# Kernel tuning notes

Measured on AMD Instinct MI355X. Metric: run time of the kernel, lower is better.

Reference implementation:

```python
import jax, jax.numpy as jnp
import numpy as np
from jax import lax


def conv2d(x, w, b, pad):
    # x: NCHW, w: OIHW
    out = lax.conv_general_dilated(x, w, (1, 1), [(pad, pad), (pad, pad)],
                                   dimension_numbers=('NCHW', 'OIHW', 'NCHW'))
    return out + b[None, :, None, None]


def traj_grid_sample(ps, gx, gy):
    """Faithful F.grid_sample (5D, trilinear, zeros padding, align_corners=False)
    applied to ps expanded along a depth axis of size L. Since every depth slice
    of the expanded input equals ps, we gather 2D from ps and fold the z-axis
    interpolation weights / bounds mask in analytically (no (B,C,L,H,W) expand).
    ps: (B,C,H,W); gx, gy: (B,L,H,W) pixel-coordinate flow fields."""
    B, C, H, W = ps.shape
    L = gx.shape[1]
    dt = ps.dtype
    # the original normalizes to [-1,1] assuming align_corners-style ranges
    gxn = gx / (W - 1) * 2 - 1
    gyn = gy / (H - 1) * 2 - 1
    gzn = jnp.arange(1, L + 1, dtype=dt) / (L - 1) * 2 - 1  # (L,)
    # torch grid_sample default align_corners=False unnormalization
    ix = ((gxn + 1) * W - 1) / 2
    iy = ((gyn + 1) * H - 1) / 2
    iz = jnp.broadcast_to((((gzn + 1) * L - 1) / 2)[None, :, None, None], ix.shape)
    x0 = jnp.floor(ix)
    y0 = jnp.floor(iy)
    z0 = jnp.floor(iz)
    bidx = jnp.arange(B)[:, None, None, None]
    out = jnp.zeros((B, L, H, W, C), dtype=dt)
    for dz in (0.0, 1.0):
        zc = z0 + dz
        wz = 1.0 - jnp.abs(iz - zc)
        mz = (zc >= 0) & (zc <= L - 1)
        for dy in (0.0, 1.0):
            yc = y0 + dy
            wy = 1.0 - jnp.abs(iy - yc)
            my = (yc >= 0) & (yc <= H - 1)
            yci = jnp.clip(yc, 0, H - 1).astype(jnp.int32)
            for dx in (0.0, 1.0):
                xc = x0 + dx
                wx = 1.0 - jnp.abs(ix - xc)
                mx = (xc >= 0) & (xc <= W - 1)
                xci = jnp.clip(xc, 0, W - 1).astype(jnp.int32)
                w = wz * wy * wx * (mz & my & mx).astype(dt)  # (B,L,H,W)
                val = ps[bidx, :, yci, xci]  # (B,L,H,W,C)
                out = out + val * w[..., None]
    return jnp.transpose(out, (0, 4, 1, 2, 3))  # (B,C,L,H,W)


def reference(x, prev_state, sub_w1, sub_b1, sub_w2, sub_b2,
              reset_w, reset_b, update_w, update_b, out_w, out_b,
              reset_ww, reset_wb, update_ww, update_wb, out_ww, out_wb):
    B, Ch, H, W = prev_state.shape
    L = sub_w2.shape[0] // 2
    # subCNN: flow generation
    s = jnp.concatenate([x, prev_state], axis=1)
    o = jax.nn.relu(conv2d(s, sub_w1, sub_b1, 2))
    o = jax.nn.relu(conv2d(o, sub_w2, sub_b2, 2))
    M = traj_grid_sample(prev_state, o[:, :L], o[:, L:])  # (B,Ch,L,H,W)
    Mf = M.reshape(B, Ch * L, H, W)  # view(B, C*L, H, W)
    update = jax.nn.sigmoid(conv2d(x, update_w, update_b, 1) + conv2d(Mf, update_ww, update_wb, 0))
    reset = jax.nn.sigmoid(conv2d(x, reset_w, reset_b, 1) + conv2d(Mf, reset_ww, reset_wb, 0))
    v = conv2d(x, out_w, out_b, 1) + reset * conv2d(Mf, out_ww, out_wb, 0)
    out_inputs = jnp.where(v >= 0, v, 0.2 * v)  # leaky_relu(0.2)
    return prev_state * update + out_inputs * (1.0 - update)


def setup_inputs() -> dict:
    key = jax.random.key(0)
    ks = jax.random.split(key, 12)
    B, Cin, Ch, L, H, W = 4, 8, 96, 13, 96, 96
    rn = lambda k, shape, s=0.05: jax.random.normal(k, shape, dtype=jnp.float32) * s
    z = lambda n: jnp.zeros((n,), jnp.float32)
    return {
        'x': rn(ks[0], (B, Cin, H, W), 1.0),
        'prev_state': rn(ks[1], (B, Ch, H, W), 1.0),
        'sub_w1': rn(ks[2], (32, Cin + Ch, 5, 5)), 'sub_b1': z(32),
        'sub_w2': rn(ks[3], (2 * L, 32, 5, 5)), 'sub_b2': z(2 * L),
        'reset_w': rn(ks[4], (Ch, Cin, 3, 3)), 'reset_b': z(Ch),
        'update_w': rn(ks[5], (Ch, Cin, 3, 3)), 'update_b': z(Ch),
        'out_w': rn(ks[6], (Ch, Cin, 3, 3)), 'out_b': z(Ch),
        'reset_ww': rn(ks[7], (Ch, Ch * L, 1, 1)), 'reset_wb': z(Ch),
        'update_ww': rn(ks[8], (Ch, Ch * L, 1, 1)), 'update_wb': z(Ch),
        'out_ww': rn(ks[9], (Ch, Ch * L, 1, 1)), 'out_wb': z(Ch),
    }
```

## Files before the change

### kernel.cpp

```cpp
#include <hip/hip_runtime.h>
#include <hip/hip_bf16.h>

#define HW 9216

typedef unsigned short ushort;
typedef unsigned int   uint;
typedef __attribute__((ext_vector_type(4))) float f32x4;
typedef __attribute__((ext_vector_type(2))) uint  u32x2;
typedef __attribute__((ext_vector_type(4))) uint  u32x4;
typedef __attribute__((ext_vector_type(4))) int   i32x4;
typedef __attribute__((ext_vector_type(8))) short s16x8;
typedef __attribute__((ext_vector_type(8))) _Float16 f16x8;

__device__ float  g_o1[4*32*HW];
__device__ float  g_q [2*4*26*HW];
__device__ __align__(16) _Float16 g_hh[4*(size_t)HW*96];
__device__ __align__(16) ushort g_chi[4*(size_t)HW*128];
__device__ __align__(16) ushort g_clo[4*(size_t)HW*128];
__device__ __align__(16) ushort g_w1b[28*4*2048];
__device__ __align__(16) ushort g_b[18*39*512];
__device__ __align__(16) float  g_urv[2304*288*16];

__device__ __forceinline__ ushort f2b(float f){
  uint x = __float_as_uint(f);
  return (ushort)((x + 0x7FFFu + ((x >> 16) & 1u)) >> 16);
}
__device__ __forceinline__ float b2f(ushort h){
  return __uint_as_float(((uint)h) << 16);
}

__global__ void pack_b_k(const float* __restrict__ uww, const float* __restrict__ rww,
                         const float* __restrict__ vww){
  int i = blockIdx.x*256 + threadIdx.x;
  if (i >= 3*96*1248) return;
  int gate = i / (96*1248); int rem = i % (96*1248);
  int oc = rem / 1248;      int kp = rem % 1248;
  int l = kp / 96, c = kp % 96;
  const float* src = (gate == 0) ? uww : ((gate == 1) ? rww : vww);
  float v = src[oc*1248 + c*13 + l];
  int n  = gate*96 + oc;
  int nt = n >> 4, nl = n & 15;
  int kb = kp >> 5, kk = kp & 31;
  g_b[(nt*39 + kb)*512 + ((kk >> 3)*16 + nl)*8 + (kk & 7)] = f2b(v);
}

__global__ void pack_w1b_k(const float* __restrict__ w1){
  int i = blockIdx.x*256 + threadIdx.x;
  if (i >= 25*4*1024) return;
  int tap = i >> 12;
  int cb  = (i >> 10) & 3;
  int oc  = (i >> 5) & 31;
  int kk  = i & 31;
  int ci  = cb*32 + kk;
  float w = (ci < 104) ? w1[oc*2600 + ci*25 + tap] : 0.f;
  ushort h = f2b(w);
  float rem = w - b2f(h);
  int base = ((tap*4 + cb) << 11) + (oc >> 4)*512 + (oc & 15)*32 + kk;
  g_w1b[base]        = h;
  g_w1b[base + 1024] = f2b(rem);
}

__global__ __launch_bounds__(256) void transpose_k(const float* __restrict__ hp,
                                                   const float* __restrict__ x){
  __shared__ float tile[32][33];
  int s0 = blockIdx.x*32;
  int b  = blockIdx.z;
  int t  = threadIdx.x;
  if (blockIdx.y < 3){
    int c0 = blockIdx.y*32;
    for (int i = t; i < 32*32; i += 256){
      int c = i >> 5, s = i & 31;
      tile[c][s] = hp[((size_t)(b*96 + c0 + c))*HW + s0 + s];
    }
    __syncthreads();
    for (int i = t; i < 32*32; i += 256){
      int s = i >> 5, c = i & 31;
      float v = tile[c][s];
      size_t px = (size_t)b*HW + s0 + s;
      g_hh[px*96 + c0 + c] = (_Float16)v;
      ushort h = f2b(v);
      g_chi[px*128 + 8 + c0 + c] = h;
      g_clo[px*128 + 8 + c0 + c] = f2b(v - b2f(h));
    }
  } else {
    for (int i = t; i < 8*32; i += 256){
      int c = i >> 5, s = i & 31;
      tile[c][s] = x[((size_t)(b*8 + c))*HW + s0 + s];
    }
    __syncthreads();
    for (int i = t; i < 32*8; i += 256){
      int s = i >> 3, c = i & 7;
      float v = tile[c][s];
      size_t px = (size_t)b*HW + s0 + s;
      ushort h = f2b(v);
      g_chi[px*128 + c] = h;
      g_clo[px*128 + c] = f2b(v - b2f(h));
    }
  }
}

__global__ __launch_bounds__(256) void conv1_mfma_k(const float* __restrict__ b1){
  __shared__ __align__(16) ushort sh[2*160*128];
  int t = threadIdx.x;
  int w = t >> 6, lane = t & 63;
  int nl = lane & 15, q = lane >> 4;
  int rt = blockIdx.x / 6, ct = blockIdx.x % 6;
  int b  = blockIdx.z;
  int r0 = rt*4, c0 = ct*16;
  const size_t pbase = (size_t)b*HW;

  #pragma unroll
  for (int i = 0; i < 20; i++){
    int idx = i*256 + t;
    int half = (i >= 10) ? 1 : 0;
    int rem = idx - half*2560;
    int px = rem >> 4, ci = rem & 15;
    int cs = ci ^ (px & 15);
    int r = px / 20, c = px - r*20;
    int gr = r0 + r - 2, gc = c0 + c - 2;
    f32x4 v = (f32x4){0.f,0.f,0.f,0.f};
    if ((unsigned)gr < 96u && (unsigned)gc < 96u){
      const ushort* src = half ? g_clo : g_chi;
      v = *(const f32x4*)(src + ((pbase + (size_t)(gr*96 + gc)) << 7) + cs*8);
    }
    *(f32x4*)((char*)sh + (size_t)idx*16) = v;
  }
  __syncthreads();

  int kxA[7], kyA[7], tpA[7];
  #pragma unroll
  for (int i = 0; i < 7; i++){
    int tp  = 7*w + i;
    int tpc = (tp > 24) ? 24 : tp;
    kyA[i] = tpc / 5;
    kxA[i] = tpc - kyA[i]*5;
    tpA[i] = tp;
  }
  int foff = nl*32 + q*8;

  f32x4 acc[4][2];
  #pragma unroll
  for (int mr = 0; mr < 4; mr++){
    acc[mr][0] = (f32x4){0.f,0.f,0.f,0.f};
    acc[mr][1] = (f32x4){0.f,0.f,0.f,0.f};
  }

  for (int cb = 0; cb < 4; cb++){
    const ushort* bpc = g_w1b + ((size_t)cb << 11);
    s16x8 bq[3][4];
#define LOADB(slot, i) { const ushort* bp = bpc + ((size_t)tpA[i] << 13); \
    bq[slot][0] = *(const s16x8*)(bp + foff); \
    bq[slot][1] = *(const s16x8*)(bp + 512 + foff); \
    bq[slot][2] = *(const s16x8*)(bp + 1024 + foff); \
    bq[slot][3] = *(const s16x8*)(bp + 1536 + foff); }
    LOADB(0, 0); LOADB(1, 1);

    #pragma unroll
    for (int i = 0; i < 7; i++){
      if (i < 5) LOADB((i + 2) % 3, i + 2);
      int ky = kyA[i], kx = kxA[i];
      int chq = cb*4 + q;
      s16x8 ah[4], al[4];
      #pragma unroll
      for (int mr = 0; mr < 4; mr++){
        int px  = (mr + ky)*20 + kx + nl;
        int off = px*256 + (((chq ^ (px & 15))) << 4);
        ah[mr] = *(const s16x8*)((const char*)sh + off);
        al[mr] = *(const s16x8*)((const char*)sh + 40960 + off);
      }
      const int cur = i % 3;
      #pragma unroll
      for (int mr = 0; mr < 4; mr++){
        acc[mr][0] = __builtin_amdgcn_mfma_f32_16x16x32_bf16(ah[mr], bq[cur][0], acc[mr][0], 0,0,0);
        acc[mr][1] = __builtin_amdgcn_mfma_f32_16x16x32_bf16(ah[mr], bq[cur][1], acc[mr][1], 0,0,0);
      }
      #pragma unroll
      for (int mr = 0; mr < 4; mr++){
        acc[mr][0] = __builtin_amdgcn_mfma_f32_16x16x32_bf16(al[mr], bq[cur][0], acc[mr][0], 0,0,0);
        acc[mr][1] = __builtin_amdgcn_mfma_f32_16x16x32_bf16(al[mr], bq[cur][1], acc[mr][1], 0,0,0);
      }
      #pragma unroll
      for (int mr = 0; mr < 4; mr++){
        acc[mr][0] = __builtin_amdgcn_mfma_f32_16x16x32_bf16(ah[mr], bq[cur][2], acc[mr][0], 0,0,0);
        acc[mr][1] = __builtin_amdgcn_mfma_f32_16x16x32_bf16(ah[mr], bq[cur][3], acc[mr][1], 0,0,0);
      }
    }
#undef LOADB
  }

  __syncthreads();
  float* red = (float*)sh;
  #pragma unroll
  for (int mr = 0; mr < 4; mr++)
    #pragma unroll
    for (int nt = 0; nt < 2; nt++)
      *(f32x4*)&red[(((mr*2 + nt)*4 + w) << 8) + lane*4] = acc[mr][nt];
  __syncthreads();

  int mr = w;
  #pragma unroll
  for (int nt = 0; nt < 2; nt++){
    f32x4 s = (f32x4){0.f,0.f,0.f,0.f};
    #pragma unroll
    for (int ww = 0; ww < 4; ww++)
      s += *(f32x4*)&red[(((mr*2 + nt)*4 + ww) << 8) + lane*4];
    int oc = nt*16 + nl;
    float bias = b1[oc];
    s.x = fmaxf(s.x + bias, 0.f); s.y = fmaxf(s.y + bias, 0.f);
    s.z = fmaxf(s.z + bias, 0.f); s.w = fmaxf(s.w + bias, 0.f);
    *(f32x4*)(g_o1 + ((size_t)(b*32 + oc))*HW + (size_t)(r0 + mr)*96 + c0 + q*4) = s;
  }
}

__global__ __launch_bounds__(256) void conv2_k(const float* __restrict__ wt2,
                                               const float* __restrict__ b2){
  __shared__ __align__(16) float in_sh[8][20][24];
  __shared__ __align__(16) float w_sh[8][25][32];
  int tile = blockIdx.x;
  int kg   = blockIdx.y;
  int b    = blockIdx.z;
  int row0 = (tile / 6) * 16, col0 = (tile % 6) * 16;
  int t = threadIdx.x;
  int og  = t >> 5;
  int pos = t & 31;
  int row = pos >> 1, x0 = (pos & 1)*8;

  float acc[8][4];
  #pragma unroll
  for (int j = 0; j < 8; j++)
    #pragma unroll
    for (int o = 0; o < 4; o++) acc[j][o] = 0.f;

  for (int cc = 0; cc < 2; cc++){
    __syncthreads();
    for (int idx = t; idx < 8*20*24; idx += 256){
      int i = idx / 480, rem = idx % 480;
      int r = rem / 24, c = rem % 24;
      int gr = row0 + r - 2, gc = col0 + c - 2;
      float v = 0.f;
      if ((unsigned)gr < 96u && (unsigned)gc < 96u){
        int ci = kg*16 + cc*8 + i;
        v = g_o1[(b*32 + ci)*HW + gr*96 + gc];
      }
      in_sh[i][r][c] = v;
    }
    for (int idx = t; idx < 8*25*32; idx += 256){
      int i = idx / 800, rem = idx % 800;
      int tap = rem / 32, oc = rem % 32;
      int ci = kg*16 + cc*8 + i;
      w_sh[i][tap][oc] = (oc < 26) ? wt2[oc*800 + ci*25 + tap] : 0.f;
    }
    __syncthreads();

    for (int i = 0; i < 8; i++){
      #pragma unroll
      for (int ky = 0; ky < 5; ky++){
        const float* rp = &in_sh[i][row + ky][x0];
        f32x4 s0 = *(const f32x4*)(rp);
        f32x4 s1 = *(const f32x4*)(rp + 4);
        f32x4 s2 = *(const f32x4*)(rp + 8);
        float seg[12] = {s0.x,s0.y,s0.z,s0.w, s1.x,s1.y,s1.z,s1.w, s2.x,s2.y,s2.z,s2.w};
        #pragma unroll
        for (int kx = 0; kx < 5; kx++){
          f32x4 wv = *(const f32x4*)&w_sh[i][ky*5 + kx][og*4];
          #pragma unroll
          for (int j = 0; j < 8; j++){
            float a = seg[kx + j];
            acc[j][0] += a*wv.x; acc[j][1] += a*wv.y;
            acc[j][2] += a*wv.z; acc[j][3] += a*wv.w;
          }
        }
      }
    }
  }

  int rg = row0 + row, cg = col0 + x0;
  #pragma unroll
  for (int o = 0; o < 4; o++){
    int slot = og*4 + o;
    if (slot < 26){
      float bias = (kg == 0) ? b2[slot] : 0.f;
      float* d = g_q + (size_t)kg*4*26*HW + ((size_t)(b*26 + slot))*HW + rg*96 + cg;
      #pragma unroll
      for (int j = 0; j < 8; j++) d[j] = acc[j][o] + bias;
    }
  }
}

__global__ __launch_bounds__(256) void gemm_k(){
  __shared__ __align__(16) ushort Bsh[18*512];
  __shared__ __align__(16) float cw4[12][64][4];
  __shared__ __align__(16) int   co4[12][64][4];
  int t = threadIdx.x;
  int w = t >> 6, lane = t & 63;
  int nl = lane & 15, quad = lane >> 4;
  int blk = blockIdx.x;
  int b   = blk / 144;
  int pbase0 = (blk % 144) * 64;
  int pt  = blk*4 + w;

  const int NQ = 4*26*HW;
  for (int idx = t; idx < 768; idx += 256){
    int l = idx >> 6, m = idx & 63;
    int p = pbase0 + m;
    float gx = fmaxf(g_q[(b*26 + l     )*HW + p] + g_q[NQ + (b*26 + l     )*HW + p], 0.f);
    float gy = fmaxf(g_q[(b*26 + 13 + l)*HW + p] + g_q[NQ + (b*26 + 13 + l)*HW + p], 0.f);
    float ix = gx * (96.f/95.f) - 0.5f;
    float iy = gy * (96.f/95.f) - 0.5f;
    float iz = (float)(l+1) * (13.f/12.f) - 0.5f;
    float z0 = floorf(iz);
    float zf = 0.f;
    #pragma unroll
    for (int dz = 0; dz < 2; dz++){
      float zc = z0 + (float)dz;
      float wz = 1.f - fabsf(iz - zc);
      if (zc >= 0.f && zc <= 12.f) zf += wz;
    }
    float x0f = floorf(ix), y0f = floorf(iy);
    #pragma unroll
    for (int dy = 0; dy < 2; dy++){
      float yc = y0f + (float)dy;
      float wy = 1.f - fabsf(iy - yc);
      bool  my = (yc >= 0.f) && (yc <= 95.f);
      int  yci = min(max((int)yc, 0), 95);
      #pragma unroll
      for (int dx = 0; dx < 2; dx++){
        float xc = x0f + (float)dx;
        float wx = 1.f - fabsf(ix - xc);
        bool  mx = (xc >= 0.f) && (xc <= 95.f);
        int  xci = min(max((int)xc, 0), 95);
        cw4[l][m][dy*2+dx] = (mx && my) ? zf*wy*wx : 0.f;
        co4[l][m][dy*2+dx] = yci*96 + xci;
      }
    }
  }

  f32x4 acc[18];
  #pragma unroll
  for (int nt = 0; nt < 18; nt++) acc[nt] = (f32x4){0.f,0.f,0.f,0.f};

  const u32x2* Bg8 = reinterpret_cast<const u32x2*>(g_b);
  const _Float16* hb = g_hh + (size_t)b*HW*96 + quad*8;
  int mloc = w*16 + nl;

  f16x8 gA[4], gB[4];
  f32x4 wA, wB;
  u32x2 sA[9], sB[9];

  #pragma unroll
  for (int u = 0; u < 9; u++){
    int idx8 = u*256 + t;
    sA[u] = Bg8[((idx8 >> 7)*39 + 0)*128 + (idx8 & 127)];
  }
  __syncthreads();

  {
    wA = *(const f32x4*)cw4[0][mloc];
    i32x4 ov_ = *(const i32x4*)co4[0][mloc];
    gA[0] = *(const f16x8*)(hb + (size_t)ov_.x*96);
    gA[1] = *(const f16x8*)(hb + (size_t)ov_.y*96);
    gA[2] = *(const f16x8*)(hb + (size_t)ov_.z*96);
    gA[3] = *(const f16x8*)(hb + (size_t)ov_.w*96);
  }
  int ln = 0, k3n = 1;

#define BODY(KB, GC, WC, GN, WN, SC, SN, PF) { \
  if (PF){ \
    _Pragma("unroll") \
    for (int u = 0; u < 9; u++){ \
      int idx8 = u*256 + t; \
      SN[u] = Bg8[((idx8 >> 7)*39 + (KB) + 1)*128 + (idx8 & 127)]; \
    } \
    WN = *(const f32x4*)cw4[ln][mloc]; \
    i32x4 ov_ = *(const i32x4*)co4[ln][mloc]; \
    const _Float16* hc_ = hb + k3n*32; \
    GN[0] = *(const f16x8*)(hc_ + (size_t)ov_.x*96); \
    GN[1] = *(const f16x8*)(hc_ + (size_t)ov_.y*96); \
    GN[2] = *(const f16x8*)(hc_ + (size_t)ov_.z*96); \
    GN[3] = *(const f16x8*)(hc_ + (size_t)ov_.w*96); \
    k3n++; if (k3n == 3){ k3n = 0; ln++; } \
  } \
  _Pragma("unroll") \
  for (int u = 0; u < 9; u++){ \
    int idx8 = u*256 + t; \
    *(u32x2*)((char*)Bsh + idx8*8) = SC[u]; \
  } \
  float av[8]; \
  _Pragma("unroll") \
  for (int j = 0; j < 8; j++) \
    av[j] = WC.x*(float)GC[0][j] + WC.y*(float)GC[1][j] \
          + WC.z*(float)GC[2][j] + WC.w*(float)GC[3][j]; \
  union { u32x4 u4; s16x8 s8v; } cv_; \
  cv_.u4.x = (uint)f2b(av[0]) | ((uint)f2b(av[1]) << 16); \
  cv_.u4.y = (uint)f2b(av[2]) | ((uint)f2b(av[3]) << 16); \
  cv_.u4.z = (uint)f2b(av[4]) | ((uint)f2b(av[5]) << 16); \
  cv_.u4.w = (uint)f2b(av[6]) | ((uint)f2b(av[7]) << 16); \
  asm volatile("s_waitcnt lgkmcnt(0)" ::: "memory"); \
  __builtin_amdgcn_s_barrier(); \
  asm volatile("" ::: "memory"); \
  _Pragma("unroll") \
  for (int nt = 0; nt < 18; nt++){ \
    s16x8 bf = *(const s16x8*)((const char*)Bsh + nt*1024 + lane*16); \
    acc[nt] = __builtin_amdgcn_mfma_f32_16x16x32_bf16(cv_.s8v, bf, acc[nt], 0, 0, 0); \
  } \
  asm volatile("" ::: "memory"); \
  __builtin_amdgcn_s_barrier(); \
  asm volatile("" ::: "memory"); \
}

  for (int kb = 0; kb < 34; kb += 2){
    BODY(kb,     gA, wA, gB, wB, sA, sB, 1);
    BODY(kb + 1, gB, wB, gA, wA, sB, sA, 1);
  }
  BODY(34, gA, wA, gB, wB, sA, sB, 1);
  BODY(35, gB, wB, gA, wA, sB, sA, 0);
#undef BODY

  float* dst = g_urv + (size_t)pt*4608;
  #pragma unroll
  for (int nt = 0; nt < 18; nt++)
    *(f32x4*)&dst[(nt*16 + nl)*16 + quad*4] = acc[nt];
}

__global__ __launch_bounds__(256) void gate_k(const float* __restrict__ x,
                        const float* __restrict__ hp,
                        const float* __restrict__ uw, const float* __restrict__ ub,
                        const float* __restrict__ rw, const float* __restrict__ rb,
                        const float* __restrict__ vw, const float* __restrict__ vb,
                        const float* __restrict__ uwb, const float* __restrict__ rwb,
                        const float* __restrict__ vwb, float* __restrict__ out){
  int p  = blockIdx.x*256 + threadIdx.x;
  int oc = blockIdx.y;
  int b  = blockIdx.z;
  int h = p/96, w = p%96;
  float xU = ub[oc], xR = rb[oc], xV = vb[oc];
  const float* xb = x + b*8*HW;
  for (int ky = 0; ky < 3; ky++){
    int r = h+ky-1;
    if ((unsigned)r >= 96u) continue;
    for (int kx = 0; kx < 3; kx++){
      int c = w+kx-1;
      if ((unsigned)c >= 96u) continue;
      int off = r*96 + c;
      int wo  = ky*3 + kx;
      #pragma unroll
      for (int ic = 0; ic < 8; ic++){
        float a = xb[ic*HW + off];
        xU += a * uw[oc*72 + ic*9 + wo];
        xR += a * rw[oc*72 + ic*9 + wo];
        xV += a * vw[oc*72 + ic*9 + wo];
      }
    }
  }
  int pt = b*576 + (p >> 4), px = p & 15;
  const float* ur = g_urv + (size_t)pt*4608 + px;
  float gU = ur[(0*96 + oc)*16] + uwb[oc];
  float gR = ur[(1*96 + oc)*16] + rwb[oc];
  float gV = ur[(2*96 + oc)*16] + vwb[oc];
  float u = 1.f / (1.f + __expf(-(xU + gU)));
  float r = 1.f / (1.f + __expf(-(xR + gR)));
  float v = xV + r * gV;
  float oi = (v >= 0.f) ? v : 0.2f*v;
  float h0 = hp[(b*96 + oc)*HW + p];
  out[(b*96 + oc)*HW + p] = h0*u + oi*(1.f - u);
}

extern "C" void kernel_launch(void* const* d_in, const int* in_sizes, int n_in,
                              void* d_out, int out_size, void* d_ws, size_t ws_size,
                              hipStream_t stream){
  const float* x    = (const float*)d_in[0];
  const float* hp   = (const float*)d_in[1];
  const float* sw1  = (const float*)d_in[2];
  const float* sb1  = (const float*)d_in[3];
  const float* sw2  = (const float*)d_in[4];
  const float* sb2  = (const float*)d_in[5];
  const float* rw   = (const float*)d_in[6];
  const float* rb   = (const float*)d_in[7];
  const float* uw   = (const float*)d_in[8];
  const float* ub   = (const float*)d_in[9];
  const float* vw   = (const float*)d_in[10];
  const float* vb   = (const float*)d_in[11];
  const float* rww  = (const float*)d_in[12];
  const float* rwb  = (const float*)d_in[13];
  const float* uww  = (const float*)d_in[14];
  const float* uwb  = (const float*)d_in[15];
  const float* vww  = (const float*)d_in[16];
  const float* vwb  = (const float*)d_in[17];

  pack_b_k    <<<dim3((3*96*1248 + 255)/256), dim3(256), 0, stream>>>(uww, rww, vww);
  pack_w1b_k  <<<dim3((25*4*1024 + 255)/256), dim3(256), 0, stream>>>(sw1);
  transpose_k <<<dim3(288, 4, 4), dim3(256), 0, stream>>>(hp, x);
  conv1_mfma_k<<<dim3(144, 1, 4), dim3(256), 0, stream>>>(sb1);
  conv2_k     <<<dim3(36, 2, 4), dim3(256), 0, stream>>>(sw2, sb2);
  gemm_k      <<<dim3(576),      dim3(256), 0, stream>>>();
  gate_k      <<<dim3(36, 96, 4), dim3(256), 0, stream>>>(x, hp,
               uw, ub, rw, rb, vw, vb, uwb, rwb, vwb, (float*)d_out);
}
```

Baseline: 346.0 us.

## Load B fragments directly from global into registers, drop LDS staging

The gemm kernel no longer stages the weight tile through shared memory with two barriers per k-step. Each wave now reads its 18 B fragments straight from global memory (L2/L1 cached) into registers at the top of each step. This removes LDS writes, LDS reads and barriers, but each of the four waves now fetches the full B tile redundantly, and the loads are no longer prefetched one step ahead, so their latency may be exposed before the MFMAs.

New measurement: 372.7 us. 7.7% more time.

```diff
diff --git a/kernel.cpp b/kernel.cpp
--- a/kernel.cpp
+++ b/kernel.cpp
@@ -288,7 +288,6 @@
 }
 
 __global__ __launch_bounds__(256) void gemm_k(){
-  __shared__ __align__(16) ushort Bsh[18*512];
   __shared__ __align__(16) float cw4[12][64][4];
   __shared__ __align__(16) int   co4[12][64][4];
   int t = threadIdx.x;
@@ -334,25 +333,18 @@
       }
     }
   }
+  __syncthreads();
 
   f32x4 acc[18];
   #pragma unroll
   for (int nt = 0; nt < 18; nt++) acc[nt] = (f32x4){0.f,0.f,0.f,0.f};
 
-  const u32x2* Bg8 = reinterpret_cast<const u32x2*>(g_b);
+  const s16x8* Bf = reinterpret_cast<const s16x8*>(g_b);
   const _Float16* hb = g_hh + (size_t)b*HW*96 + quad*8;
   int mloc = w*16 + nl;
 
   f16x8 gA[4], gB[4];
   f32x4 wA, wB;
-  u32x2 sA[9], sB[9];
-
-  #pragma unroll
-  for (int u = 0; u < 9; u++){
-    int idx8 = u*256 + t;
-    sA[u] = Bg8[((idx8 >> 7)*39 + 0)*128 + (idx8 & 127)];
-  }
-  __syncthreads();
 
   {
     wA = *(const f32x4*)cw4[0][mloc];
@@ -364,13 +356,11 @@
   }
   int ln = 0, k3n = 1;
 
-#define BODY(KB, GC, WC, GN, WN, SC, SN, PF) { \
+#define BODY(KB, GC, WC, GN, WN, PF) { \
+  s16x8 bq[18]; \
+  _Pragma("unroll") \
+  for (int nt = 0; nt < 18; nt++) bq[nt] = Bf[(nt*39 + (KB))*64 + lane]; \
   if (PF){ \
-    _Pragma("unroll") \
-    for (int u = 0; u < 9; u++){ \
-      int idx8 = u*256 + t; \
-      SN[u] = Bg8[((idx8 >> 7)*39 + (KB) + 1)*128 + (idx8 & 127)]; \
-    } \
     WN = *(const f32x4*)cw4[ln][mloc]; \
     i32x4 ov_ = *(const i32x4*)co4[ln][mloc]; \
     const _Float16* hc_ = hb + k3n*32; \
@@ -379,11 +369,6 @@
     GN[2] = *(const f16x8*)(hc_ + (size_t)ov_.z*96); \
     GN[3] = *(const f16x8*)(hc_ + (size_t)ov_.w*96); \
     k3n++; if (k3n == 3){ k3n = 0; ln++; } \
-  } \
-  _Pragma("unroll") \
-  for (int u = 0; u < 9; u++){ \
-    int idx8 = u*256 + t; \
-    *(u32x2*)((char*)Bsh + idx8*8) = SC[u]; \
   } \
   float av[8]; \
   _Pragma("unroll") \
@@ -395,25 +380,17 @@
   cv_.u4.y = (uint)f2b(av[2]) | ((uint)f2b(av[3]) << 16); \
   cv_.u4.z = (uint)f2b(av[4]) | ((uint)f2b(av[5]) << 16); \
   cv_.u4.w = (uint)f2b(av[6]) | ((uint)f2b(av[7]) << 16); \
-  asm volatile("s_waitcnt lgkmcnt(0)" ::: "memory"); \
-  __builtin_amdgcn_s_barrier(); \
-  asm volatile("" ::: "memory"); \
   _Pragma("unroll") \
-  for (int nt = 0; nt < 18; nt++){ \
-    s16x8 bf = *(const s16x8*)((const char*)Bsh + nt*1024 + lane*16); \
-    acc[nt] = __builtin_amdgcn_mfma_f32_16x16x32_bf16(cv_.s8v, bf, acc[nt], 0, 0, 0); \
-  } \
-  asm volatile("" ::: "memory"); \
-  __builtin_amdgcn_s_barrier(); \
-  asm volatile("" ::: "memory"); \
+  for (int nt = 0; nt < 18; nt++) \
+    acc[nt] = __builtin_amdgcn_mfma_f32_16x16x32_bf16(cv_.s8v, bq[nt], acc[nt], 0, 0, 0); \
 }
 
   for (int kb = 0; kb < 34; kb += 2){
-    BODY(kb,     gA, wA, gB, wB, sA, sB, 1);
-    BODY(kb + 1, gB, wB, gA, wA, sB, sA, 1);
-  }
-  BODY(34, gA, wA, gB, wB, sA, sB, 1);
-  BODY(35, gB, wB, gA, wA, sB, sA, 0);
+    BODY(kb,     gA, wA, gB, wB, 1);
+    BODY(kb + 1, gB, wB, gA, wA, 1);
+  }
+  BODY(34, gA, wA, gB, wB, 1);
+  BODY(35, gB, wB, gA, wA, 0);
 #undef BODY
 
   float* dst = g_urv + (size_t)pt*4608;
```
